# Kernel optimization log

Hardware: AMD Instinct MI355X
Metric: run time of the kernel (lower is better)

Reference implementation:

```python
import jax, jax.numpy as jnp
import numpy as np

B, S, D, E, TOP_K = 4, 4096, 2048, 64, 2


def setup_inputs() -> dict:
    key = jax.random.key(0)
    kx, kw, kb = jax.random.split(key, 3)
    x = jax.random.normal(kx, (B, S, D), dtype=jnp.float32)
    # nn.Linear(d_model, n_expert): weight (E, D), bias (E,)
    bound = 1.0 / np.sqrt(D)
    W = jax.random.uniform(kw, (E, D), dtype=jnp.float32, minval=-bound, maxval=bound)
    b = jax.random.uniform(kb, (E,), dtype=jnp.float32, minval=-bound, maxval=bound)
    return {"x": x, "W": W, "b": b}


def reference(x, W, b):
    # logits: (B, S, E)
    logits = jnp.einsum("bsd,ed->bse", x, W) + b
    top_k_logits, ids = jax.lax.top_k(logits, TOP_K)  # (B,S,K) each
    # scatter top-k logits into a -inf filled tensor along the expert dim
    n = B * S
    flat = jnp.full((n, E), -jnp.inf, dtype=logits.dtype)
    rows = jnp.arange(n)[:, None]  # (n,1)
    flat = flat.at[rows, ids.reshape(n, TOP_K)].set(top_k_logits.reshape(n, TOP_K))
    sparse_logits = flat.reshape(B, S, E)
    router_output = jax.nn.softmax(sparse_logits, axis=-1)  # zeros outside top-k
    return router_output, ids
```

## Files before the change

kernel.cpp:

```cpp
#include <hip/hip_runtime.h>
#include <math.h>

#define NTOK 16384
#define D_   2048
#define E_   64
#define TPB  64
#define NKC  (D_/32)
#define NCH  32

typedef _Float16 f16x8 __attribute__((ext_vector_type(8)));
typedef float    f32x4 __attribute__((ext_vector_type(4)));

#define LSCALE      256.0f
#define LSCALE2_INV (1.0f/65536.0f)

#define SMEM_FLOATS 32768

__global__ __launch_bounds__(256)
void prep_w(const float* __restrict__ W,
            _Float16* __restrict__ wh, _Float16* __restrict__ wl)
{
    const int idx = blockIdx.x * 256 + threadIdx.x;
    const int l  = idx & 63;
    const int kc = (idx >> 6) & 63;
    const int nt = idx >> 12;
    const int e  = nt * 16 + (l & 15);
    const int g  = l >> 4;
    const float* src = W + (size_t)e * D_ + kc * 32 + g * 4;
    const float4 f0 = *reinterpret_cast<const float4*>(src);
    const float4 f1 = *reinterpret_cast<const float4*>(src + 16);
    const float v[8] = {f0.x, f0.y, f0.z, f0.w, f1.x, f1.y, f1.z, f1.w};
    f16x8 h, lo;
#pragma unroll
    for (int j = 0; j < 8; ++j) {
        const float vs = v[j] * LSCALE;
        const _Float16 hj = (_Float16)vs;
        h[j]  = hj;
        lo[j] = (_Float16)(vs - (float)hj);
    }
    *reinterpret_cast<f16x8*>(wh + (size_t)idx * 8) = h;
    *reinterpret_cast<f16x8*>(wl + (size_t)idx * 8) = lo;
}

__device__ __forceinline__ void stage16(const void* g, void* l) {
    __builtin_amdgcn_global_load_lds(
        (const __attribute__((address_space(1))) void*)g,
        (__attribute__((address_space(3))) void*)l, 16, 0, 0);
}

__global__ __launch_bounds__(256, 1)
void router_mfma(const float* __restrict__ x,
                 const _Float16* __restrict__ wh,
                 const _Float16* __restrict__ wl,
                 const float* __restrict__ bias,
                 float* __restrict__ out)
{
    __shared__ float smem[SMEM_FLOATS];
    char* sb = (char*)smem;

    const int tid = threadIdx.x;
    const int l   = tid & 63;
    const int w   = __builtin_amdgcn_readfirstlane(tid >> 6);
    const int T0  = blockIdx.x * TPB;
    const int g   = l >> 4;

    f32x4 acc0 = {0.f,0.f,0.f,0.f}, acc1 = {0.f,0.f,0.f,0.f};
    f32x4 acc2 = {0.f,0.f,0.f,0.f}, acc3 = {0.f,0.f,0.f,0.f};

    const int rlo   = l >> 3;
    const int sslot = (l & 7) ^ (rlo & 7);
    const float* xs0 = x + (size_t)(T0 + w*16 + 0 + rlo) * D_ + sslot * 4;
    const float* xs1 = x + (size_t)(T0 + w*16 + 8 + rlo) * D_ + sslot * 4;
    const _Float16* bhs = wh + (size_t)w * NKC * 512 / 8 * 8;
    const _Float16* bls = wl + (size_t)w * NKC * 512;
    const _Float16* bhs_ = wh + (size_t)w * NKC * 512;

    auto STAGE = [&](int c) {
        char* bb = sb + (size_t)(c & 3) * 32768;
        const int kc0 = c * 2;
#pragma unroll
        for (int p = 0; p < 2; ++p) {
            const int kc = kc0 + p;
            stage16(xs0 + (size_t)kc * 32, bb + p*8192 + (w*16 + 0) * 128);
            stage16(xs1 + (size_t)kc * 32, bb + p*8192 + (w*16 + 8) * 128);
            stage16(bhs_ + (size_t)kc * 512 + l * 8,
                    bb + 16384 + p*8192 + w*2048);
            stage16(bls  + (size_t)kc * 512 + l * 8,
                    bb + 16384 + p*8192 + w*2048 + 1024);
        }
    };

    const int trow   = w*16 + (l & 15);
    const int t7     = trow & 7;
    const int xa_off = trow * 128 + ((g       ^ t7) << 4);
    const int xb_off = trow * 128 + (((4 + g) ^ t7) << 4);

    auto COMPUTE = [&](int c) {
        const char* bb = sb + (size_t)(c & 3) * 32768;
#pragma unroll
        for (int p = 0; p < 2; ++p) {
            const float4 xa = *reinterpret_cast<const float4*>(bb + p*8192 + xa_off);
            const float4 xb = *reinterpret_cast<const float4*>(bb + p*8192 + xb_off);
            const char* bp = bb + 16384 + p*8192;
            const f16x8 bh0 = *reinterpret_cast<const f16x8*>(bp + 0*2048 +        (l << 4));
            const f16x8 bl0 = *reinterpret_cast<const f16x8*>(bp + 0*2048 + 1024 + (l << 4));
            const f16x8 bh1 = *reinterpret_cast<const f16x8*>(bp + 1*2048 +        (l << 4));
            const f16x8 bl1 = *reinterpret_cast<const f16x8*>(bp + 1*2048 + 1024 + (l << 4));
            const f16x8 bh2 = *reinterpret_cast<const f16x8*>(bp + 2*2048 +        (l << 4));
            const f16x8 bl2 = *reinterpret_cast<const f16x8*>(bp + 2*2048 + 1024 + (l << 4));
            const f16x8 bh3 = *reinterpret_cast<const f16x8*>(bp + 3*2048 +        (l << 4));
            const f16x8 bl3 = *reinterpret_cast<const f16x8*>(bp + 3*2048 + 1024 + (l << 4));
            f16x8 ah, al_;
            {
                float vs;
                vs = xa.x * LSCALE; ah[0] = (_Float16)vs; al_[0] = (_Float16)(vs - (float)ah[0]);
                vs = xa.y * LSCALE; ah[1] = (_Float16)vs; al_[1] = (_Float16)(vs - (float)ah[1]);
                vs = xa.z * LSCALE; ah[2] = (_Float16)vs; al_[2] = (_Float16)(vs - (float)ah[2]);
                vs = xa.w * LSCALE; ah[3] = (_Float16)vs; al_[3] = (_Float16)(vs - (float)ah[3]);
                vs = xb.x * LSCALE; ah[4] = (_Float16)vs; al_[4] = (_Float16)(vs - (float)ah[4]);
                vs = xb.y * LSCALE; ah[5] = (_Float16)vs; al_[5] = (_Float16)(vs - (float)ah[5]);
                vs = xb.z * LSCALE; ah[6] = (_Float16)vs; al_[6] = (_Float16)(vs - (float)ah[6]);
                vs = xb.w * LSCALE; ah[7] = (_Float16)vs; al_[7] = (_Float16)(vs - (float)ah[7]);
            }
            acc0 = __builtin_amdgcn_mfma_f32_16x16x32_f16(ah,  bh0, acc0, 0, 0, 0);
            acc0 = __builtin_amdgcn_mfma_f32_16x16x32_f16(al_, bh0, acc0, 0, 0, 0);
            acc0 = __builtin_amdgcn_mfma_f32_16x16x32_f16(ah,  bl0, acc0, 0, 0, 0);
            acc1 = __builtin_amdgcn_mfma_f32_16x16x32_f16(ah,  bh1, acc1, 0, 0, 0);
            acc1 = __builtin_amdgcn_mfma_f32_16x16x32_f16(al_, bh1, acc1, 0, 0, 0);
            acc1 = __builtin_amdgcn_mfma_f32_16x16x32_f16(ah,  bl1, acc1, 0, 0, 0);
            acc2 = __builtin_amdgcn_mfma_f32_16x16x32_f16(ah,  bh2, acc2, 0, 0, 0);
            acc2 = __builtin_amdgcn_mfma_f32_16x16x32_f16(al_, bh2, acc2, 0, 0, 0);
            acc2 = __builtin_amdgcn_mfma_f32_16x16x32_f16(ah,  bl2, acc2, 0, 0, 0);
            acc3 = __builtin_amdgcn_mfma_f32_16x16x32_f16(ah,  bh3, acc3, 0, 0, 0);
            acc3 = __builtin_amdgcn_mfma_f32_16x16x32_f16(al_, bh3, acc3, 0, 0, 0);
            acc3 = __builtin_amdgcn_mfma_f32_16x16x32_f16(ah,  bl3, acc3, 0, 0, 0);
        }
    };

    STAGE(0); STAGE(1); STAGE(2);
    for (int c = 0; c < NCH; ++c) {
        if (c <= NCH - 3)      { asm volatile("s_waitcnt vmcnt(16)" ::: "memory"); }
        else if (c == NCH - 2) { asm volatile("s_waitcnt vmcnt(8)"  ::: "memory"); }
        else                   { asm volatile("s_waitcnt vmcnt(0)"  ::: "memory"); }
        __builtin_amdgcn_s_barrier();
        if (c + 3 < NCH) STAGE(c + 3);
        __builtin_amdgcn_sched_barrier(0);
        COMPUTE(c);
    }

    {
        float* logits = smem;
        const int col = l & 15;
#pragma unroll
        for (int r = 0; r < 4; ++r) {
            const int t = w*16 + g * 4 + r;
            logits[t * 65 + 0  + col] = acc0[r] * LSCALE2_INV;
            logits[t * 65 + 16 + col] = acc1[r] * LSCALE2_INV;
            logits[t * 65 + 32 + col] = acc2[r] * LSCALE2_INV;
            logits[t * 65 + 48 + col] = acc3[r] * LSCALE2_INV;
        }
    }
    __syncthreads();

    float* res = smem + TPB * 65;
    if (tid < TPB) {
        const float* lg = smem + tid * 65;
        float m1 = -INFINITY, m2 = -INFINITY;
        int i1 = 0, i2 = 0;
        for (int e = 0; e < E_; ++e) {
            const float v = lg[e] + bias[e];
            if (v > m1)      { m2 = m1; i2 = i1; m1 = v; i1 = e; }
            else if (v > m2) { m2 = v;  i2 = e; }
        }
        const float ex  = expf(m2 - m1);
        const float den = 1.f + ex;
        res[tid*4+0] = 1.f / den;
        res[tid*4+1] = ex / den;
        res[tid*4+2] = (float)i1;
        res[tid*4+3] = (float)i2;
    }
    __syncthreads();

    float* ob = out + (size_t)T0 * E_;
#pragma unroll
    for (int i = 0; i < 4; ++i) {
        const int idx = i * 1024 + tid * 4;
        const int t   = idx >> 6;
        const int e0  = idx & 63;
        const float p1 = res[t*4+0];
        const float p2 = res[t*4+1];
        const int   i1 = (int)res[t*4+2];
        const int   i2 = (int)res[t*4+3];
        float4 v;
        v.x = (e0+0 == i1) ? p1 : ((e0+0 == i2) ? p2 : 0.f);
        v.y = (e0+1 == i1) ? p1 : ((e0+1 == i2) ? p2 : 0.f);
        v.z = (e0+2 == i1) ? p1 : ((e0+2 == i2) ? p2 : 0.f);
        v.w = (e0+3 == i1) ? p1 : ((e0+3 == i2) ? p2 : 0.f);
        *reinterpret_cast<float4*>(ob + idx) = v;
    }
    if (tid < TPB * 2) {
        out[(size_t)NTOK * E_ + (size_t)T0 * 2 + tid] =
            res[(tid >> 1) * 4 + 2 + (tid & 1)];
    }
}

extern "C" void kernel_launch(void* const* d_in, const int* in_sizes, int n_in,
                              void* d_out, int out_size, void* d_ws, size_t ws_size,
                              hipStream_t stream) {
    const float* x = (const float*)d_in[0];
    const float* W = (const float*)d_in[1];
    const float* b = (const float*)d_in[2];
    float* out     = (float*)d_out;
    _Float16* wh   = (_Float16*)d_ws;
    _Float16* wl   = wh + (size_t)4 * NKC * 64 * 8;

    hipLaunchKernelGGL(prep_w, dim3(64), dim3(256), 0, stream, W, wh, wl);
    hipLaunchKernelGGL(router_mfma, dim3(NTOK / TPB), dim3(256), 0, stream,
                       x, wh, wl, b, out);
}
```

Baseline: 56.13 us.

## Give each wave a private 3-deep LDS ring to drop block barriers

Replaces the block-shared 4-buffer LDS pipeline, which split x and W staging across waves and needed an s_barrier every chunk, with a per-wave 3-slot ring. Each wave now stages its own 16 x rows plus all four expert tiles of the hi/lo fp16 weights. It waits only on its own vmcnt, so the main loop has no block-wide synchronisation. The cost is that every wave fetches the full weight slice, which multiplies weight traffic from L2 by four per block, and the prefetch depth drops from 3 chunks of 2 k-slices to 2 k-slices.

```diff
diff --git a/kernel.cpp b/kernel.cpp
--- a/kernel.cpp
+++ b/kernel.cpp
@@ -6,7 +6,6 @@
 #define E_   64
 #define TPB  64
 #define NKC  (D_/32)
-#define NCH  32
 
 typedef _Float16 f16x8 __attribute__((ext_vector_type(8)));
 typedef float    f32x4 __attribute__((ext_vector_type(4)));
@@ -14,7 +13,10 @@
 #define LSCALE      256.0f
 #define LSCALE2_INV (1.0f/65536.0f)
 
-#define SMEM_FLOATS 32768
+#define PAGE_B      10240
+#define DEPTH       3
+#define WAVE_B      (DEPTH * PAGE_B)
+#define SMEM_FLOATS (4 * WAVE_B / 4)
 
 __global__ __launch_bounds__(256)
 void prep_w(const float* __restrict__ W,
@@ -63,97 +65,101 @@
     const int w   = __builtin_amdgcn_readfirstlane(tid >> 6);
     const int T0  = blockIdx.x * TPB;
     const int g   = l >> 4;
+    char* wb = sb + w * WAVE_B;
 
     f32x4 acc0 = {0.f,0.f,0.f,0.f}, acc1 = {0.f,0.f,0.f,0.f};
     f32x4 acc2 = {0.f,0.f,0.f,0.f}, acc3 = {0.f,0.f,0.f,0.f};
 
-    const int rlo   = l >> 3;
-    const int sslot = (l & 7) ^ (rlo & 7);
-    const float* xs0 = x + (size_t)(T0 + w*16 + 0 + rlo) * D_ + sslot * 4;
-    const float* xs1 = x + (size_t)(T0 + w*16 + 8 + rlo) * D_ + sslot * 4;
-    const _Float16* bhs = wh + (size_t)w * NKC * 512 / 8 * 8;
-    const _Float16* bls = wl + (size_t)w * NKC * 512;
-    const _Float16* bhs_ = wh + (size_t)w * NKC * 512;
-
-    auto STAGE = [&](int c) {
-        char* bb = sb + (size_t)(c & 3) * 32768;
-        const int kc0 = c * 2;
-#pragma unroll
-        for (int p = 0; p < 2; ++p) {
-            const int kc = kc0 + p;
-            stage16(xs0 + (size_t)kc * 32, bb + p*8192 + (w*16 + 0) * 128);
-            stage16(xs1 + (size_t)kc * 32, bb + p*8192 + (w*16 + 8) * 128);
-            stage16(bhs_ + (size_t)kc * 512 + l * 8,
-                    bb + 16384 + p*8192 + w*2048);
-            stage16(bls  + (size_t)kc * 512 + l * 8,
-                    bb + 16384 + p*8192 + w*2048 + 1024);
+    const int rlo = l >> 3;
+    const int ssl = (l & 7) ^ rlo;
+    const float* xsA = x + (size_t)(T0 + w * 16 + rlo) * D_ + ssl * 4;
+    const float* xsB = xsA + (size_t)8 * D_;
+    const _Float16* bh_b = wh + (size_t)l * 8;
+    const _Float16* bl_b = wl + (size_t)l * 8;
+
+    auto STAGE = [&](int kc, int slot) {
+        char* pg = wb + slot * PAGE_B;
+        stage16(xsA + (size_t)kc * 32, pg);
+        stage16(xsB + (size_t)kc * 32, pg + 1024);
+#pragma unroll
+        for (int nt = 0; nt < 4; ++nt) {
+            stage16(bh_b + nt * 32768 + (size_t)kc * 512, pg + 2048 + nt * 2048);
+            stage16(bl_b + nt * 32768 + (size_t)kc * 512, pg + 2048 + nt * 2048 + 1024);
         }
     };
 
-    const int trow   = w*16 + (l & 15);
+    const int trow   = l & 15;
     const int t7     = trow & 7;
     const int xa_off = trow * 128 + ((g       ^ t7) << 4);
     const int xb_off = trow * 128 + (((4 + g) ^ t7) << 4);
 
-    auto COMPUTE = [&](int c) {
-        const char* bb = sb + (size_t)(c & 3) * 32768;
-#pragma unroll
-        for (int p = 0; p < 2; ++p) {
-            const float4 xa = *reinterpret_cast<const float4*>(bb + p*8192 + xa_off);
-            const float4 xb = *reinterpret_cast<const float4*>(bb + p*8192 + xb_off);
-            const char* bp = bb + 16384 + p*8192;
-            const f16x8 bh0 = *reinterpret_cast<const f16x8*>(bp + 0*2048 +        (l << 4));
-            const f16x8 bl0 = *reinterpret_cast<const f16x8*>(bp + 0*2048 + 1024 + (l << 4));
-            const f16x8 bh1 = *reinterpret_cast<const f16x8*>(bp + 1*2048 +        (l << 4));
-            const f16x8 bl1 = *reinterpret_cast<const f16x8*>(bp + 1*2048 + 1024 + (l << 4));
-            const f16x8 bh2 = *reinterpret_cast<const f16x8*>(bp + 2*2048 +        (l << 4));
-            const f16x8 bl2 = *reinterpret_cast<const f16x8*>(bp + 2*2048 + 1024 + (l << 4));
-            const f16x8 bh3 = *reinterpret_cast<const f16x8*>(bp + 3*2048 +        (l << 4));
-            const f16x8 bl3 = *reinterpret_cast<const f16x8*>(bp + 3*2048 + 1024 + (l << 4));
-            f16x8 ah, al_;
-            {
-                float vs;
-                vs = xa.x * LSCALE; ah[0] = (_Float16)vs; al_[0] = (_Float16)(vs - (float)ah[0]);
-                vs = xa.y * LSCALE; ah[1] = (_Float16)vs; al_[1] = (_Float16)(vs - (float)ah[1]);
-                vs = xa.z * LSCALE; ah[2] = (_Float16)vs; al_[2] = (_Float16)(vs - (float)ah[2]);
-                vs = xa.w * LSCALE; ah[3] = (_Float16)vs; al_[3] = (_Float16)(vs - (float)ah[3]);
-                vs = xb.x * LSCALE; ah[4] = (_Float16)vs; al_[4] = (_Float16)(vs - (float)ah[4]);
-                vs = xb.y * LSCALE; ah[5] = (_Float16)vs; al_[5] = (_Float16)(vs - (float)ah[5]);
-                vs = xb.z * LSCALE; ah[6] = (_Float16)vs; al_[6] = (_Float16)(vs - (float)ah[6]);
-                vs = xb.w * LSCALE; ah[7] = (_Float16)vs; al_[7] = (_Float16)(vs - (float)ah[7]);
-            }
-            acc0 = __builtin_amdgcn_mfma_f32_16x16x32_f16(ah,  bh0, acc0, 0, 0, 0);
-            acc0 = __builtin_amdgcn_mfma_f32_16x16x32_f16(al_, bh0, acc0, 0, 0, 0);
-            acc0 = __builtin_amdgcn_mfma_f32_16x16x32_f16(ah,  bl0, acc0, 0, 0, 0);
-            acc1 = __builtin_amdgcn_mfma_f32_16x16x32_f16(ah,  bh1, acc1, 0, 0, 0);
-            acc1 = __builtin_amdgcn_mfma_f32_16x16x32_f16(al_, bh1, acc1, 0, 0, 0);
-            acc1 = __builtin_amdgcn_mfma_f32_16x16x32_f16(ah,  bl1, acc1, 0, 0, 0);
-            acc2 = __builtin_amdgcn_mfma_f32_16x16x32_f16(ah,  bh2, acc2, 0, 0, 0);
-            acc2 = __builtin_amdgcn_mfma_f32_16x16x32_f16(al_, bh2, acc2, 0, 0, 0);
-            acc2 = __builtin_amdgcn_mfma_f32_16x16x32_f16(ah,  bl2, acc2, 0, 0, 0);
-            acc3 = __builtin_amdgcn_mfma_f32_16x16x32_f16(ah,  bh3, acc3, 0, 0, 0);
-            acc3 = __builtin_amdgcn_mfma_f32_16x16x32_f16(al_, bh3, acc3, 0, 0, 0);
-            acc3 = __builtin_amdgcn_mfma_f32_16x16x32_f16(ah,  bl3, acc3, 0, 0, 0);
-        }
+    auto COMPUTE = [&](int slot) {
+        const char* pg = wb + slot * PAGE_B;
+        const float4 xa = *reinterpret_cast<const float4*>(pg + xa_off);
+        const float4 xb = *reinterpret_cast<const float4*>(pg + xb_off);
+        const f16x8 bh0 = *reinterpret_cast<const f16x8*>(pg + 2048 + 0*2048 +        (l << 4));
+        const f16x8 bl0 = *reinterpret_cast<const f16x8*>(pg + 2048 + 0*2048 + 1024 + (l << 4));
+        const f16x8 bh1 = *reinterpret_cast<const f16x8*>(pg + 2048 + 1*2048 +        (l << 4));
+        const f16x8 bl1 = *reinterpret_cast<const f16x8*>(pg + 2048 + 1*2048 + 1024 + (l << 4));
+        const f16x8 bh2 = *reinterpret_cast<const f16x8*>(pg + 2048 + 2*2048 +        (l << 4));
+        const f16x8 bl2 = *reinterpret_cast<const f16x8*>(pg + 2048 + 2*2048 + 1024 + (l << 4));
+        const f16x8 bh3 = *reinterpret_cast<const f16x8*>(pg + 2048 + 3*2048 +        (l << 4));
+        const f16x8 bl3 = *reinterpret_cast<const f16x8*>(pg + 2048 + 3*2048 + 1024 + (l << 4));
+        f16x8 ah, al_;
+        {
+            float vs;
+            vs = xa.x * LSCALE; ah[0] = (_Float16)vs; al_[0] = (_Float16)(vs - (float)ah[0]);
+            vs = xa.y * LSCALE; ah[1] = (_Float16)vs; al_[1] = (_Float16)(vs - (float)ah[1]);
+            vs = xa.z * LSCALE; ah[2] = (_Float16)vs; al_[2] = (_Float16)(vs - (float)ah[2]);
+            vs = xa.w * LSCALE; ah[3] = (_Float16)vs; al_[3] = (_Float16)(vs - (float)ah[3]);
+            vs = xb.x * LSCALE; ah[4] = (_Float16)vs; al_[4] = (_Float16)(vs - (float)ah[4]);
+            vs = xb.y * LSCALE; ah[5] = (_Float16)vs; al_[5] = (_Float16)(vs - (float)ah[5]);
+            vs = xb.z * LSCALE; ah[6] = (_Float16)vs; al_[6] = (_Float16)(vs - (float)ah[6]);
+            vs = xb.w * LSCALE; ah[7] = (_Float16)vs; al_[7] = (_Float16)(vs - (float)ah[7]);
+        }
+        acc0 = __builtin_amdgcn_mfma_f32_16x16x32_f16(ah,  bh0, acc0, 0, 0, 0);
+        acc0 = __builtin_amdgcn_mfma_f32_16x16x32_f16(al_, bh0, acc0, 0, 0, 0);
+        acc0 = __builtin_amdgcn_mfma_f32_16x16x32_f16(ah,  bl0, acc0, 0, 0, 0);
+        acc1 = __builtin_amdgcn_mfma_f32_16x16x32_f16(ah,  bh1, acc1, 0, 0, 0);
+        acc1 = __builtin_amdgcn_mfma_f32_16x16x32_f16(al_, bh1, acc1, 0, 0, 0);
+        acc1 = __builtin_amdgcn_mfma_f32_16x16x32_f16(ah,  bl1, acc1, 0, 0, 0);
+        acc2 = __builtin_amdgcn_mfma_f32_16x16x32_f16(ah,  bh2, acc2, 0, 0, 0);
+        acc2 = __builtin_amdgcn_mfma_f32_16x16x32_f16(al_, bh2, acc2, 0, 0, 0);
+        acc2 = __builtin_amdgcn_mfma_f32_16x16x32_f16(ah,  bl2, acc2, 0, 0, 0);
+        acc3 = __builtin_amdgcn_mfma_f32_16x16x32_f16(ah,  bh3, acc3, 0, 0, 0);
+        acc3 = __builtin_amdgcn_mfma_f32_16x16x32_f16(al_, bh3, acc3, 0, 0, 0);
+        acc3 = __builtin_amdgcn_mfma_f32_16x16x32_f16(ah,  bl3, acc3, 0, 0, 0);
     };
 
-    STAGE(0); STAGE(1); STAGE(2);
-    for (int c = 0; c < NCH; ++c) {
-        if (c <= NCH - 3)      { asm volatile("s_waitcnt vmcnt(16)" ::: "memory"); }
-        else if (c == NCH - 2) { asm volatile("s_waitcnt vmcnt(8)"  ::: "memory"); }
-        else                   { asm volatile("s_waitcnt vmcnt(0)"  ::: "memory"); }
-        __builtin_amdgcn_s_barrier();
-        if (c + 3 < NCH) STAGE(c + 3);
-        __builtin_amdgcn_sched_barrier(0);
-        COMPUTE(c);
-    }
+#define KSTEP(KC, CSLOT, SSLOT)                                          \
+    do {                                                                 \
+        asm volatile("s_waitcnt vmcnt(10)" ::: "memory");                \
+        __builtin_amdgcn_sched_barrier(0);                               \
+        if ((KC) + 2 < NKC) STAGE((KC) + 2, (SSLOT));                    \
+        __builtin_amdgcn_sched_barrier(0);                               \
+        COMPUTE(CSLOT);                                                  \
+    } while (0)
+
+    STAGE(0, 0); STAGE(1, 1);
+    for (int m = 0; m < 21; ++m) {
+        const int kc = m * 3;
+        KSTEP(kc + 0, 0, 2);
+        KSTEP(kc + 1, 1, 0);
+        KSTEP(kc + 2, 2, 1);
+    }
+    asm volatile("s_waitcnt vmcnt(0)" ::: "memory");
+    __builtin_amdgcn_sched_barrier(0);
+    COMPUTE(0);
+#undef KSTEP
+
+    __syncthreads();
 
     {
         float* logits = smem;
         const int col = l & 15;
 #pragma unroll
         for (int r = 0; r < 4; ++r) {
-            const int t = w*16 + g * 4 + r;
+            const int t = w * 16 + g * 4 + r;
             logits[t * 65 + 0  + col] = acc0[r] * LSCALE2_INV;
             logits[t * 65 + 16 + col] = acc1[r] * LSCALE2_INV;
             logits[t * 65 + 32 + col] = acc2[r] * LSCALE2_INV;
```

After: 61.76 us. 1.1x slower.
